# Kernel tuning notes

Hardware: AMD Instinct MI355X
Metric: run time of the kernel (lower is better)

The kernel has to match this reference:

```python
import jax, jax.numpy as jnp
import numpy as np

OUT = 7       # roi_pooling_output_size
SR = 2        # bilinear samples per bin side (torchvision default is adaptive; fixed here)
STRIDES = (4, 8, 16, 32)
LEVELS = (2, 3, 4, 5)  # log2(strides)


def _roi_align(feat, boxes, bidx, scale):
    """roi_align, aligned=False. feat [B,C,H,W], boxes [N,4] xyxy image coords."""
    N = boxes.shape[0]
    C, H, W = feat.shape[1], feat.shape[2], feat.shape[3]
    x1 = boxes[:, 0] * scale; y1 = boxes[:, 1] * scale
    x2 = boxes[:, 2] * scale; y2 = boxes[:, 3] * scale
    rw = jnp.maximum(x2 - x1, 1.0); rh = jnp.maximum(y2 - y1, 1.0)
    g = (jnp.arange(SR, dtype=feat.dtype) + 0.5) / SR
    off = (jnp.arange(OUT, dtype=feat.dtype)[:, None] + g[None, :]).reshape(-1)  # [OUT*SR]
    ys = y1[:, None] + off[None, :] * (rh / OUT)[:, None]  # [N, OUT*SR]
    xs = x1[:, None] + off[None, :] * (rw / OUT)[:, None]
    M = OUT * SR
    y = jnp.broadcast_to(ys[:, :, None], (N, M, M)).reshape(N, M * M)
    x = jnp.broadcast_to(xs[:, None, :], (N, M, M)).reshape(N, M * M)
    valid = (y > -1.0) & (y < H) & (x > -1.0) & (x < W)
    y = jnp.clip(y, 0.0, H - 1); x = jnp.clip(x, 0.0, W - 1)
    y0f = jnp.floor(y); x0f = jnp.floor(x)
    y0 = y0f.astype(jnp.int32); x0 = x0f.astype(jnp.int32)
    yb = jnp.minimum(y0 + 1, H - 1); xb = jnp.minimum(x0 + 1, W - 1)
    ly = y - y0f; lx = x - x0f

    def gat(yi, xi):
        return feat[bidx[:, None], :, yi, xi]  # [N, P, C]

    v = (((1 - ly) * (1 - lx))[..., None] * gat(y0, x0)
         + ((1 - ly) * lx)[..., None] * gat(y0, xb)
         + (ly * (1 - lx))[..., None] * gat(yb, x0)
         + (ly * lx)[..., None] * gat(yb, xb))
    v = jnp.where(valid[..., None], v, 0.0)
    v = v.reshape(N, OUT, SR, OUT, SR, C).mean(axis=(2, 4))  # avg samples per bin
    return v.transpose(0, 3, 1, 2)  # [N, C, OUT, OUT]


def _forward(feat2, feat3, feat4, feat5, rois, W_fc1, b_fc1, W_fc2, b_fc2,
             W_cls, b_cls, W_reg, b_reg):
    feats = (feat2, feat3, feat4, feat5)
    BS, R = rois.shape[0], rois.shape[1]
    N = BS * R
    boxes = rois.reshape(N, 4)
    bidx = jnp.repeat(jnp.arange(BS, dtype=jnp.int32), R)
    w = boxes[:, 2] - boxes[:, 0]
    h = boxes[:, 3] - boxes[:, 1]
    # FPN level routing: floor(4 + log2(sqrt(wh)/224 + 1e-6)); unclamped, as in source
    lv = jnp.floor(4.0 + jnp.log2(jnp.sqrt(w * h) / 224.0 + 1e-6))
    C = feat2.shape[1]
    roi_feats = jnp.zeros((N, C, OUT, OUT), dtype=feat2.dtype)
    for f, s, l in zip(feats, STRIDES, LEVELS):
        rf = _roi_align(f, boxes, bidx, 1.0 / s)
        roi_feats = roi_feats + jnp.where((lv == l)[:, None, None, None], rf, 0.0)
    x = roi_feats.reshape(N, -1)                    # [N, 12544]
    x = jax.nn.relu(x @ W_fc1.T + b_fc1)            # roi_head fc1
    x = jax.nn.relu(x @ W_fc2.T + b_fc2)            # roi_head fc2
    cls_pred = (x @ W_cls.T + b_cls).reshape(BS, R, -1)
    reg_pred = (x @ W_reg.T + b_reg).reshape(BS, R, -1, 4)
    return cls_pred, reg_pred


def setup_inputs() -> dict:
    key = jax.random.key(0)
    ks = jax.random.split(key, 12)
    BS, R, C = 2, 512, 256
    IMG = 800.0
    inp = {}
    for i, (name, s) in enumerate(zip(['feat2', 'feat3', 'feat4', 'feat5'],
                                      [200, 100, 50, 25])):
        inp[name] = jax.random.normal(ks[i], (BS, C, s, s), dtype=jnp.float32)
    # realistic ROIs: uniform centers, log-uniform sizes in [32, 512] px
    ctr = jax.random.uniform(ks[4], (BS, R, 2), minval=0.0, maxval=IMG)
    sz = jnp.exp(jax.random.uniform(ks[5], (BS, R, 2),
                                    minval=jnp.log(32.0), maxval=jnp.log(512.0)))
    x1y1 = jnp.clip(ctr - sz / 2, 0.0, IMG)
    x2y2 = jnp.clip(ctr + sz / 2, 0.0, IMG)
    inp['rois'] = jnp.concatenate([x1y1, x2y2], axis=-1)
    D, F, NCLS = 1024, C * OUT * OUT, 80
    inp['W_fc1'] = 0.01 * jax.random.normal(ks[6], (D, F), dtype=jnp.float32)
    inp['b_fc1'] = jnp.zeros((D,), dtype=jnp.float32)
    inp['W_fc2'] = 0.01 * jax.random.normal(ks[7], (D, D), dtype=jnp.float32)
    inp['b_fc2'] = jnp.zeros((D,), dtype=jnp.float32)
    inp['W_cls'] = 0.01 * jax.random.normal(ks[8], (NCLS + 1, D), dtype=jnp.float32)
    inp['b_cls'] = jnp.zeros((NCLS + 1,), dtype=jnp.float32)
    inp['W_reg'] = 0.01 * jax.random.normal(ks[9], (NCLS * 4, D), dtype=jnp.float32)
    inp['b_reg'] = jnp.zeros((NCLS * 4,), dtype=jnp.float32)
    return inp


def reference(feat2, feat3, feat4, feat5, rois, W_fc1, b_fc1, W_fc2, b_fc2,
              W_cls, b_cls, W_reg, b_reg):
    return _forward(feat2, feat3, feat4, feat5, rois, W_fc1, b_fc1, W_fc2, b_fc2,
                    W_cls, b_cls, W_reg, b_reg)
```

## Files before the change

### kernel.cpp

```cpp
#include <hip/hip_runtime.h>

typedef __bf16 bf16_t;
typedef __bf16 bf16x8 __attribute__((ext_vector_type(8)));
typedef __bf16 bf16x4v __attribute__((ext_vector_type(4)));
typedef float f32x4 __attribute__((ext_vector_type(4)));

#define GLDS16(g, l)                                                            \
  __builtin_amdgcn_global_load_lds((const __attribute__((address_space(1))) void*)(g), \
                                   (__attribute__((address_space(3))) void*)(l), 16, 0, 0)

__global__ __launch_bounds__(256) void prep_all(const float* __restrict__ f2,
                                                const float* __restrict__ f3,
                                                const float* __restrict__ f4,
                                                const float* __restrict__ f5,
                                                const float* __restrict__ W1,
                                                const float* __restrict__ W2,
                                                const float* __restrict__ Wc,
                                                const float* __restrict__ bc,
                                                const float* __restrict__ Wr,
                                                const float* __restrict__ br,
                                                bf16_t* __restrict__ FT2,
                                                bf16_t* __restrict__ FT3,
                                                bf16_t* __restrict__ FT4,
                                                bf16_t* __restrict__ FT5,
                                                bf16_t* __restrict__ W1p,
                                                bf16_t* __restrict__ W2b,
                                                bf16_t* __restrict__ Wcb,
                                                float* __restrict__ bcat) {
  __shared__ __align__(16) char smraw[25344];
  const int bid = blockIdx.x;
  const int t = threadIdx.x;

  if (bid < 6656) {
    float* tile = (float*)smraw;
    const float* src; bf16_t* dst; int P, rel, ptiles;
    if (bid < 5000)      { src = f2; dst = FT2; P = 40000; rel = bid;        ptiles = 625; }
    else if (bid < 6256) { src = f3; dst = FT3; P = 10000; rel = bid - 5000; ptiles = 157; }
    else if (bid < 6576) { src = f4; dst = FT4; P = 2500;  rel = bid - 6256; ptiles = 40; }
    else                 { src = f5; dst = FT5; P = 625;   rel = bid - 6576; ptiles = 10; }
    const int pt = rel % ptiles;
    const int cb = (rel / ptiles) & 3;
    const int b = rel / (ptiles * 4);
    const int p0 = pt * 64, c0 = cb * 64;
    const float* s = src + (size_t)(b * 256 + c0) * P;
#pragma unroll
    for (int it = 0; it < 16; ++it) {
      const int ch = it * 4 + (t >> 6);
      const int px = t & 63;
      float v = 0.0f;
      if (p0 + px < P) v = s[(size_t)ch * P + p0 + px];
      tile[ch * 65 + px] = v;
    }
    __syncthreads();
    bf16_t* d = dst + ((size_t)b * P + p0) * 256 + c0;
#pragma unroll
    for (int it = 0; it < 4; ++it) {
      const int px = it * 16 + (t >> 4);
      const int ch4 = (t & 15) * 4;
      if (p0 + px < P) {
        union { bf16_t bb[4]; uint2 u; } pk;
#pragma unroll
        for (int k2 = 0; k2 < 4; k2++) pk.bb[k2] = (bf16_t)tile[(ch4 + k2) * 65 + px];
        *(uint2*)&d[(size_t)px * 256 + ch4] = pk.u;
      }
    }
  } else if (bid < 7680) {
    bf16_t* pw = (bf16_t*)smraw;
    const int row = bid - 6656;
    const float* src = W1 + (size_t)row * 12544;
    for (int it = 0; it < 49; ++it) {
      const int j = it * 256 + t;
      const int c = j / 49;
      const int bin = j - c * 49;
      pw[bin * 258 + c] = (bf16_t)src[j];
    }
    __syncthreads();
    bf16_t* dst = W1p + (size_t)row * 12544;
    for (int j4 = t; j4 < 3136; j4 += 256) {
      const int bin = j4 >> 6;
      const int c = (j4 & 63) * 4;
      union { bf16_t bb[4]; uint2 u; } pk;
#pragma unroll
      for (int k2 = 0; k2 < 4; k2++) pk.bb[k2] = pw[bin * 258 + c + k2];
      ((uint2*)dst)[j4] = pk.u;
    }
  } else if (bid < 8704) {
    const int i = (bid - 7680) * 256 + t;
    float4 v = ((const float4*)W2)[i];
    union { bf16_t b[4]; uint2 u; } p;
    p.b[0] = (bf16_t)v.x; p.b[1] = (bf16_t)v.y; p.b[2] = (bf16_t)v.z; p.b[3] = (bf16_t)v.w;
    ((uint2*)W2b)[i] = p.u;
  } else {
    const int i = (bid - 8704) * 256 + t;
    const int row = i >> 10, col = i & 1023;
    float v = 0.0f;
    if (row < 81) v = Wc[row * 1024 + col];
    else if (row < 401) v = Wr[(row - 81) * 1024 + col];
    Wcb[i] = (bf16_t)v;
    if (i < 448) bcat[i] = (i < 81) ? bc[i] : ((i < 401) ? br[i - 81] : 0.0f);
  }
}

__global__ __launch_bounds__(256) void roi_align_nhwc(const bf16_t* __restrict__ fb2,
                                                      const bf16_t* __restrict__ fb3,
                                                      const bf16_t* __restrict__ fb4,
                                                      const bf16_t* __restrict__ fb5,
                                                      const float* __restrict__ rois,
                                                      bf16_t* __restrict__ A) {
  const int n = blockIdx.x;
  const int t = threadIdx.x;
  const int b = n >> 9;
  const float4 box = ((const float4*)rois)[n];
  const float w = box.z - box.x, h = box.w - box.y;
  const int lv = (int)floorf(4.0f + log2f(sqrtf(w * h) / 224.0f + 1e-6f));
  bf16_t* Ar = A + (size_t)n * 12544;

  if (lv < 2 || lv > 5) {
    uint2 z; z.x = 0; z.y = 0;
    for (int j = t; j < 3136; j += 256) ((uint2*)Ar)[j] = z;
    return;
  }

  const bf16_t* F; int H, W; float scale;
  if (lv == 2)      { F = fb2; H = 200; W = 200; scale = 0.25f; }
  else if (lv == 3) { F = fb3; H = 100; W = 100; scale = 0.125f; }
  else if (lv == 4) { F = fb4; H = 50;  W = 50;  scale = 0.0625f; }
  else              { F = fb5; H = 25;  W = 25;  scale = 0.03125f; }
  F += (size_t)b * H * W * 256;

  __shared__ int   s_x0[14], s_xb[14], s_y0w[14], s_ybw[14];
  __shared__ float s_wx0[14], s_wx1[14], s_wy0[14], s_wy1[14];

  const float x1s = box.x * scale, y1s = box.y * scale;
  const float x2s = box.z * scale, y2s = box.w * scale;
  const float rw = fmaxf(x2s - x1s, 1.0f), rh = fmaxf(y2s - y1s, 1.0f);
  const float bwx = rw * (1.0f / 7.0f), bwy = rh * (1.0f / 7.0f);

  if (t < 14) {
    const int i2 = t >> 1, j = t & 1;
    const float off = (float)i2 + ((float)j + 0.5f) * 0.5f;
    float x = x1s + off * bwx;
    float vx = (x > -1.0f && x < (float)W) ? 1.0f : 0.0f;
    x = fminf(fmaxf(x, 0.0f), (float)(W - 1));
    float x0f = floorf(x);
    int x0 = (int)x0f;
    s_x0[t] = x0; s_xb[t] = min(x0 + 1, W - 1);
    float lx = x - x0f;
    s_wx0[t] = (1.0f - lx) * vx; s_wx1[t] = lx * vx;
    float y = y1s + off * bwy;
    float vy = (y > -1.0f && y < (float)H) ? 1.0f : 0.0f;
    y = fminf(fmaxf(y, 0.0f), (float)(H - 1));
    float y0f = floorf(y);
    int y0 = (int)y0f;
    s_y0w[t] = y0 * W; s_ybw[t] = min(y0 + 1, H - 1) * W;
    float ly = y - y0f;
    s_wy0[t] = (1.0f - ly) * vy; s_wy1[t] = ly * vy;
  }
  __syncthreads();

  const int wv = t >> 6, l = t & 63;
  const int c4 = l * 4;
  for (int bin = wv; bin < 49; bin += 4) {
    const int by = bin / 7, bx = bin - by * 7;
    float a0 = 0, a1 = 0, a2 = 0, a3 = 0;
#pragma unroll
    for (int sa = 0; sa < 2; sa++) {
      const int my = 2 * by + sa;
      const int y0w = s_y0w[my], ybw = s_ybw[my];
      const float wy0 = s_wy0[my], wy1 = s_wy1[my];
#pragma unroll
      for (int sb = 0; sb < 2; sb++) {
        const int mx = 2 * bx + sb;
        const int x0 = s_x0[mx], xb = s_xb[mx];
        const float w00 = wy0 * s_wx0[mx], w01 = wy0 * s_wx1[mx];
        const float w10 = wy1 * s_wx0[mx], w11 = wy1 * s_wx1[mx];
        bf16x4v v00 = *(const bf16x4v*)&F[(size_t)(y0w + x0) * 256 + c4];
        bf16x4v v01 = *(const bf16x4v*)&F[(size_t)(y0w + xb) * 256 + c4];
        bf16x4v v10 = *(const bf16x4v*)&F[(size_t)(ybw + x0) * 256 + c4];
        bf16x4v v11 = *(const bf16x4v*)&F[(size_t)(ybw + xb) * 256 + c4];
        a0 += w00 * (float)v00[0] + w01 * (float)v01[0] + w10 * (float)v10[0] + w11 * (float)v11[0];
        a1 += w00 * (float)v00[1] + w01 * (float)v01[1] + w10 * (float)v10[1] + w11 * (float)v11[1];
        a2 += w00 * (float)v00[2] + w01 * (float)v01[2] + w10 * (float)v10[2] + w11 * (float)v11[2];
        a3 += w00 * (float)v00[3] + w01 * (float)v01[3] + w10 * (float)v10[3] + w11 * (float)v11[3];
      }
    }
    union { bf16_t bb[4]; uint2 u; } pk;
    pk.bb[0] = (bf16_t)(a0 * 0.25f);
    pk.bb[1] = (bf16_t)(a1 * 0.25f);
    pk.bb[2] = (bf16_t)(a2 * 0.25f);
    pk.bb[3] = (bf16_t)(a3 * 0.25f);
    *(uint2*)&Ar[bin * 256 + c4] = pk.u;
  }
}

__global__ __launch_bounds__(256, 2) void gemm1_splitk(const bf16_t* __restrict__ A,
                                                       const bf16_t* __restrict__ B,
                                                       float* __restrict__ Cp) {
  __shared__ __align__(16) bf16_t As[128 * 32];
  __shared__ __align__(16) bf16_t Bs[128 * 32];
  const int t = threadIdx.x;
  const int w = t >> 6, l = t & 63;
  const int bm = blockIdx.x * 128, bn = blockIdx.y * 128;
  const int K = 12544;
  const int k0 = blockIdx.z * 1568;
  const int row1 = t >> 2;
  const int kc = ((t & 3) ^ ((t >> 3) & 3)) * 8;
  const bf16_t* gA1 = A + (size_t)(bm + row1) * K + k0 + kc;
  const bf16_t* gA2 = gA1 + (size_t)64 * K;
  const bf16_t* gB1 = B + (size_t)(bn + row1) * K + k0 + kc;
  const bf16_t* gB2 = gB1 + (size_t)64 * K;
  bf16_t* lA1 = As + w * 512;
  bf16_t* lA2 = As + 2048 + w * 512;
  bf16_t* lB1 = Bs + w * 512;
  bf16_t* lB2 = Bs + 2048 + w * 512;
  const int wm = (w >> 1) * 64, wn = (w & 1) * 64;
  const int rA = l & 15;
  const int kqs = (((l >> 4) ^ ((rA >> 1) & 3))) * 8;
  f32x4 acc[4][4] = {};

  for (int kk = 0; kk < 49; ++kk) {
    GLDS16(gA1, lA1); GLDS16(gA2, lA2);
    GLDS16(gB1, lB1); GLDS16(gB2, lB2);
    gA1 += 32; gA2 += 32; gB1 += 32; gB2 += 32;
    __syncthreads();
    bf16x8 a[4], b[4];
#pragma unroll
    for (int i = 0; i < 4; i++) {
      a[i] = *(const bf16x8*)&As[(wm + i * 16 + rA) * 32 + kqs];
      b[i] = *(const bf16x8*)&Bs[(wn + i * 16 + rA) * 32 + kqs];
    }
#pragma unroll
    for (int i = 0; i < 4; i++)
#pragma unroll
      for (int j = 0; j < 4; j++)
        acc[i][j] = __builtin_amdgcn_mfma_f32_16x16x32_bf16(a[i], b[j], acc[i][j], 0, 0, 0);
    __syncthreads();
  }

  const int q = l >> 4, cc = l & 15;
  float* Co = Cp + ((size_t)blockIdx.z << 20);
#pragma unroll
  for (int i = 0; i < 4; i++)
#pragma unroll
    for (int j = 0; j < 4; j++) {
      const int col = bn + wn + j * 16 + cc;
      const int r0 = bm + wm + i * 16 + q * 4;
#pragma unroll
      for (int r = 0; r < 4; r++)
        Co[(size_t)(r0 + r) * 1024 + col] = acc[i][j][r];
    }
}

__global__ __launch_bounds__(256) void reduce_fc1(const float* __restrict__ Cp,
                                                  const float* __restrict__ bias,
                                                  bf16_t* __restrict__ X) {
  const int i4 = blockIdx.x * 256 + threadIdx.x;
  const float4* C4 = (const float4*)Cp;
  float4 s = C4[i4];
#pragma unroll
  for (int z = 1; z < 8; z++) {
    float4 v = C4[(size_t)z * 262144 + i4];
    s.x += v.x; s.y += v.y; s.z += v.z; s.w += v.w;
  }
  const float4 bv = *(const float4*)&bias[(i4 & 255) * 4];
  union { bf16_t bb[4]; uint2 u; } pk;
  pk.bb[0] = (bf16_t)fmaxf(s.x + bv.x, 0.0f);
  pk.bb[1] = (bf16_t)fmaxf(s.y + bv.y, 0.0f);
  pk.bb[2] = (bf16_t)fmaxf(s.z + bv.z, 0.0f);
  pk.bb[3] = (bf16_t)fmaxf(s.w + bv.w, 0.0f);
  ((uint2*)X)[i4] = pk.u;
}

template <int MODE>
__global__ __launch_bounds__(256) void gemm_bt(const bf16_t* __restrict__ A,
                                               const bf16_t* __restrict__ B,
                                               const float* __restrict__ bias,
                                               void* __restrict__ out,
                                               int M, int N, int K) {
  __shared__ __align__(16) bf16_t As[64 * 32];
  __shared__ __align__(16) bf16_t Bs[64 * 32];
  const int t = threadIdx.x;
  const int wv = t >> 6, l = t & 63;
  const int bm = blockIdx.x * 64, bn = blockIdx.y * 64;
  const int wm = (wv >> 1) * 32, wn = (wv & 1) * 32;

  const int srow = t >> 2;
  const int skc = (t & 3) * 8;
  const int sst = ((t & 3) ^ ((t >> 3) & 3)) * 8;
  const bf16_t* ga = A + (size_t)(bm + srow) * K + skc;
  const bf16_t* gb = B + (size_t)(bn + srow) * K + skc;

  uint4 ra = *(const uint4*)ga;
  uint4 rb = *(const uint4*)gb;
  f32x4 acc[2][2] = {};

  const int nIter = K >> 5;
  const int rA = l & 15;
  const int kqs = (((l >> 4) ^ ((rA >> 1) & 3))) * 8;
  for (int i = 0; i < nIter; ++i) {
    ga += 32; gb += 32;
    *(uint4*)&As[srow * 32 + sst] = ra;
    *(uint4*)&Bs[srow * 32 + sst] = rb;
    __syncthreads();
    if (i + 1 < nIter) { ra = *(const uint4*)ga; rb = *(const uint4*)gb; }
    bf16x8 a0 = *(const bf16x8*)&As[(wm + rA) * 32 + kqs];
    bf16x8 a1 = *(const bf16x8*)&As[(wm + 16 + rA) * 32 + kqs];
    bf16x8 b0 = *(const bf16x8*)&Bs[(wn + rA) * 32 + kqs];
    bf16x8 b1 = *(const bf16x8*)&Bs[(wn + 16 + rA) * 32 + kqs];
    acc[0][0] = __builtin_amdgcn_mfma_f32_16x16x32_bf16(a0, b0, acc[0][0], 0, 0, 0);
    acc[0][1] = __builtin_amdgcn_mfma_f32_16x16x32_bf16(a0, b1, acc[0][1], 0, 0, 0);
    acc[1][0] = __builtin_amdgcn_mfma_f32_16x16x32_bf16(a1, b0, acc[1][0], 0, 0, 0);
    acc[1][1] = __builtin_amdgcn_mfma_f32_16x16x32_bf16(a1, b1, acc[1][1], 0, 0, 0);
    __syncthreads();
  }

  const int q = l >> 4;
  const int cc = l & 15;
#pragma unroll
  for (int i2 = 0; i2 < 2; i2++) {
#pragma unroll
    for (int j2 = 0; j2 < 2; j2++) {
      const int col = bn + wn + j2 * 16 + cc;
      const int row0 = bm + wm + i2 * 16 + q * 4;
      const float bv = bias[col];
#pragma unroll
      for (int r = 0; r < 4; r++) {
        float v = acc[i2][j2][r] + bv;
        const int row = row0 + r;
        if (MODE == 0) {
          v = fmaxf(v, 0.0f);
          ((bf16_t*)out)[(size_t)row * N + col] = (bf16_t)v;
        } else {
          if (col < 81)       ((float*)out)[(size_t)row * 81 + col] = v;
          else if (col < 401) ((float*)out)[82944 + (size_t)row * 320 + (col - 81)] = v;
        }
      }
    }
  }
}

extern "C" void kernel_launch(void* const* d_in, const int* in_sizes, int n_in,
                              void* d_out, int out_size, void* d_ws, size_t ws_size,
                              hipStream_t stream) {
  const float* f2   = (const float*)d_in[0];
  const float* f3   = (const float*)d_in[1];
  const float* f4   = (const float*)d_in[2];
  const float* f5   = (const float*)d_in[3];
  const float* rois = (const float*)d_in[4];
  const float* W1   = (const float*)d_in[5];
  const float* b1   = (const float*)d_in[6];
  const float* W2   = (const float*)d_in[7];
  const float* b2   = (const float*)d_in[8];
  const float* Wc   = (const float*)d_in[9];
  const float* bc   = (const float*)d_in[10];
  const float* Wr   = (const float*)d_in[11];
  const float* br   = (const float*)d_in[12];

  char* ws = (char*)d_ws;
  bf16_t* Ab   = (bf16_t*)(ws);
  bf16_t* W1b  = (bf16_t*)(ws + 25690112);
  bf16_t* X1b  = (bf16_t*)(ws + 51380224);
  bf16_t* W2b  = (bf16_t*)(ws + 53477376);
  bf16_t* X2b  = (bf16_t*)(ws + 55574528);
  bf16_t* Wcb  = (bf16_t*)(ws + 57671680);
  float*  bcat = (float*)(ws + 58589184);
  bf16_t* FT   = (bf16_t*)(ws + 58591232);
  float*  Cp   = (float*)(ws + 58591232);
  bf16_t* FT2 = FT;
  bf16_t* FT3 = FT + 20480000;
  bf16_t* FT4 = FT + 25600000;
  bf16_t* FT5 = FT + 26880000;

  prep_all<<<10496, 256, 0, stream>>>(f2, f3, f4, f5, W1, W2, Wc, bc, Wr, br,
                                      FT2, FT3, FT4, FT5, W1b, W2b, Wcb, bcat);
  roi_align_nhwc<<<1024, 256, 0, stream>>>(FT2, FT3, FT4, FT5, rois, Ab);
  gemm1_splitk<<<dim3(8, 8, 8), 256, 0, stream>>>(Ab, W1b, Cp);
  reduce_fc1<<<1024, 256, 0, stream>>>(Cp, b1, X1b);
  gemm_bt<0><<<dim3(16, 16), 256, 0, stream>>>(X1b, W2b, b2, (void*)X2b, 1024, 1024, 1024);
  gemm_bt<1><<<dim3(16, 7), 256, 0, stream>>>(X2b, Wcb, bcat, d_out, 1024, 448, 1024);
}
```

Before: 327.0 us.

## Vectorize prep and roi_align loads, split W1 transpose, shrink gemm1 M-tile

```diff
diff --git a/kernel.cpp b/kernel.cpp
--- a/kernel.cpp
+++ b/kernel.cpp
@@ -2,7 +2,6 @@
 
 typedef __bf16 bf16_t;
 typedef __bf16 bf16x8 __attribute__((ext_vector_type(8)));
-typedef __bf16 bf16x4v __attribute__((ext_vector_type(4)));
 typedef float f32x4 __attribute__((ext_vector_type(4)));
 
 #define GLDS16(g, l)                                                            \
@@ -27,7 +26,7 @@
                                                 bf16_t* __restrict__ W2b,
                                                 bf16_t* __restrict__ Wcb,
                                                 float* __restrict__ bcat) {
-  __shared__ __align__(16) char smraw[25344];
+  __shared__ __align__(16) char smraw[16640];
   const int bid = blockIdx.x;
   const int t = threadIdx.x;
 
@@ -43,13 +42,24 @@
     const int b = rel / (ptiles * 4);
     const int p0 = pt * 64, c0 = cb * 64;
     const float* s = src + (size_t)(b * 256 + c0) * P;
-#pragma unroll
-    for (int it = 0; it < 16; ++it) {
-      const int ch = it * 4 + (t >> 6);
-      const int px = t & 63;
-      float v = 0.0f;
-      if (p0 + px < P) v = s[(size_t)ch * P + p0 + px];
-      tile[ch * 65 + px] = v;
+    if (p0 + 64 <= P && (P & 3) == 0) {
+      const int chb = t >> 4, px4 = (t & 15) * 4;
+#pragma unroll
+      for (int it = 0; it < 4; ++it) {
+        const int ch = it * 16 + chb;
+        float4 v = *(const float4*)&s[(size_t)ch * P + p0 + px4];
+        float* tr = &tile[ch * 65 + px4];
+        tr[0] = v.x; tr[1] = v.y; tr[2] = v.z; tr[3] = v.w;
+      }
+    } else {
+#pragma unroll
+      for (int it = 0; it < 16; ++it) {
+        const int ch = it * 4 + (t >> 6);
+        const int px = t & 63;
+        float v = 0.0f;
+        if (p0 + px < P) v = s[(size_t)ch * P + p0 + px];
+        tile[ch * 65 + px] = v;
+      }
     }
     __syncthreads();
     bf16_t* d = dst + ((size_t)b * P + p0) * 256 + c0;
@@ -64,40 +74,44 @@
         *(uint2*)&d[(size_t)px * 256 + ch4] = pk.u;
       }
     }
-  } else if (bid < 7680) {
-    bf16_t* pw = (bf16_t*)smraw;
-    const int row = bid - 6656;
-    const float* src = W1 + (size_t)row * 12544;
-    for (int it = 0; it < 49; ++it) {
-      const int j = it * 256 + t;
-      const int c = j / 49;
-      const int bin = j - c * 49;
-      pw[bin * 258 + c] = (bf16_t)src[j];
-    }
-    __syncthreads();
-    bf16_t* dst = W1p + (size_t)row * 12544;
-    for (int j4 = t; j4 < 3136; j4 += 256) {
-      const int bin = j4 >> 6;
-      const int c = (j4 & 63) * 4;
+  } else if (bid < 8704) {
+    bf16_t* lin = (bf16_t*)smraw;
+    const int idx = bid - 6656;
+    const int row = idx >> 1, c0 = (idx & 1) * 128;
+    const float* src = W1 + (size_t)row * 12544 + (size_t)c0 * 49;
+    for (int i = t; i < 1568; i += 256) {
+      float4 v = ((const float4*)src)[i];
       union { bf16_t bb[4]; uint2 u; } pk;
-#pragma unroll
-      for (int k2 = 0; k2 < 4; k2++) pk.bb[k2] = pw[bin * 258 + c + k2];
-      ((uint2*)dst)[j4] = pk.u;
-    }
-  } else if (bid < 8704) {
-    const int i = (bid - 7680) * 256 + t;
+      pk.bb[0] = (bf16_t)v.x; pk.bb[1] = (bf16_t)v.y;
+      pk.bb[2] = (bf16_t)v.z; pk.bb[3] = (bf16_t)v.w;
+      *(uint2*)&lin[i * 4] = pk.u;
+    }
+    __syncthreads();
+    bf16_t* dst = W1p + (size_t)row * 12544 + c0;
+    for (int j4 = t; j4 < 1568; j4 += 256) {
+      const int bin = j4 >> 5;
+      const int lc = (j4 & 31) * 4;
+      union { bf16_t bb[4]; uint2 u; } pk;
+#pragma unroll
+      for (int k2 = 0; k2 < 4; k2++) pk.bb[k2] = lin[(lc + k2) * 49 + bin];
+      *(uint2*)&dst[bin * 256 + lc] = pk.u;
+    }
+  } else if (bid < 9728) {
+    const int i = (bid - 8704) * 256 + t;
     float4 v = ((const float4*)W2)[i];
     union { bf16_t b[4]; uint2 u; } p;
     p.b[0] = (bf16_t)v.x; p.b[1] = (bf16_t)v.y; p.b[2] = (bf16_t)v.z; p.b[3] = (bf16_t)v.w;
     ((uint2*)W2b)[i] = p.u;
   } else {
-    const int i = (bid - 8704) * 256 + t;
-    const int row = i >> 10, col = i & 1023;
-    float v = 0.0f;
-    if (row < 81) v = Wc[row * 1024 + col];
-    else if (row < 401) v = Wr[(row - 81) * 1024 + col];
-    Wcb[i] = (bf16_t)v;
-    if (i < 448) bcat[i] = (i < 81) ? bc[i] : ((i < 401) ? br[i - 81] : 0.0f);
+    const int q = (bid - 9728) * 256 + t;
+    const int row = q >> 8, col4 = (q & 255) * 4;
+    float4 v = {0.0f, 0.0f, 0.0f, 0.0f};
+    if (row < 81) v = *(const float4*)&Wc[row * 1024 + col4];
+    else if (row < 401) v = *(const float4*)&Wr[(row - 81) * 1024 + col4];
+    union { bf16_t b[4]; uint2 u; } p;
+    p.b[0] = (bf16_t)v.x; p.b[1] = (bf16_t)v.y; p.b[2] = (bf16_t)v.z; p.b[3] = (bf16_t)v.w;
+    ((uint2*)Wcb)[q] = p.u;
+    if (q < 448) bcat[q] = (q < 81) ? bc[q] : ((q < 401) ? br[q - 81] : 0.0f);
   }
 }
 
@@ -116,8 +130,8 @@
   bf16_t* Ar = A + (size_t)n * 12544;
 
   if (lv < 2 || lv > 5) {
-    uint2 z; z.x = 0; z.y = 0;
-    for (int j = t; j < 3136; j += 256) ((uint2*)Ar)[j] = z;
+    uint4 z = {0, 0, 0, 0};
+    for (int j = t; j < 1568; j += 256) ((uint4*)Ar)[j] = z;
     return;
   }
 
@@ -159,10 +173,12 @@
   __syncthreads();
 
   const int wv = t >> 6, l = t & 63;
-  const int c4 = l * 4;
-  for (int bin = wv; bin < 49; bin += 4) {
+  const int half = l >> 5, c8 = (l & 31) * 8;
+  for (int p = wv; p < 25; p += 4) {
+    const int bin = 2 * p + half;
+    if (bin >= 49) continue;
     const int by = bin / 7, bx = bin - by * 7;
-    float a0 = 0, a1 = 0, a2 = 0, a3 = 0;
+    float a[8] = {};
 #pragma unroll
     for (int sa = 0; sa < 2; sa++) {
       const int my = 2 * by + sa;
@@ -174,63 +190,57 @@
         const int x0 = s_x0[mx], xb = s_xb[mx];
         const float w00 = wy0 * s_wx0[mx], w01 = wy0 * s_wx1[mx];
         const float w10 = wy1 * s_wx0[mx], w11 = wy1 * s_wx1[mx];
-        bf16x4v v00 = *(const bf16x4v*)&F[(size_t)(y0w + x0) * 256 + c4];
-        bf16x4v v01 = *(const bf16x4v*)&F[(size_t)(y0w + xb) * 256 + c4];
-        bf16x4v v10 = *(const bf16x4v*)&F[(size_t)(ybw + x0) * 256 + c4];
-        bf16x4v v11 = *(const bf16x4v*)&F[(size_t)(ybw + xb) * 256 + c4];
-        a0 += w00 * (float)v00[0] + w01 * (float)v01[0] + w10 * (float)v10[0] + w11 * (float)v11[0];
-        a1 += w00 * (float)v00[1] + w01 * (float)v01[1] + w10 * (float)v10[1] + w11 * (float)v11[1];
-        a2 += w00 * (float)v00[2] + w01 * (float)v01[2] + w10 * (float)v10[2] + w11 * (float)v11[2];
-        a3 += w00 * (float)v00[3] + w01 * (float)v01[3] + w10 * (float)v10[3] + w11 * (float)v11[3];
-      }
-    }
-    union { bf16_t bb[4]; uint2 u; } pk;
-    pk.bb[0] = (bf16_t)(a0 * 0.25f);
-    pk.bb[1] = (bf16_t)(a1 * 0.25f);
-    pk.bb[2] = (bf16_t)(a2 * 0.25f);
-    pk.bb[3] = (bf16_t)(a3 * 0.25f);
-    *(uint2*)&Ar[bin * 256 + c4] = pk.u;
-  }
-}
-
-__global__ __launch_bounds__(256, 2) void gemm1_splitk(const bf16_t* __restrict__ A,
+        bf16x8 v00 = *(const bf16x8*)&F[(size_t)(y0w + x0) * 256 + c8];
+        bf16x8 v01 = *(const bf16x8*)&F[(size_t)(y0w + xb) * 256 + c8];
+        bf16x8 v10 = *(const bf16x8*)&F[(size_t)(ybw + x0) * 256 + c8];
+        bf16x8 v11 = *(const bf16x8*)&F[(size_t)(ybw + xb) * 256 + c8];
+#pragma unroll
+        for (int k2 = 0; k2 < 8; k2++)
+          a[k2] += w00 * (float)v00[k2] + w01 * (float)v01[k2]
+                 + w10 * (float)v10[k2] + w11 * (float)v11[k2];
+      }
+    }
+    union { bf16_t bb[8]; uint4 u; } pk;
+#pragma unroll
+    for (int k2 = 0; k2 < 8; k2++) pk.bb[k2] = (bf16_t)(a[k2] * 0.25f);
+    *(uint4*)&Ar[bin * 256 + c8] = pk.u;
+  }
+}
+
+__global__ __launch_bounds__(256, 4) void gemm1_splitk(const bf16_t* __restrict__ A,
                                                        const bf16_t* __restrict__ B,
                                                        float* __restrict__ Cp) {
-  __shared__ __align__(16) bf16_t As[128 * 32];
+  __shared__ __align__(16) bf16_t As[64 * 32];
   __shared__ __align__(16) bf16_t Bs[128 * 32];
   const int t = threadIdx.x;
   const int w = t >> 6, l = t & 63;
-  const int bm = blockIdx.x * 128, bn = blockIdx.y * 128;
+  const int bm = blockIdx.x * 64, bn = blockIdx.y * 128;
   const int K = 12544;
   const int k0 = blockIdx.z * 1568;
-  const int row1 = t >> 2;
+  const int row = t >> 2;
   const int kc = ((t & 3) ^ ((t >> 3) & 3)) * 8;
-  const bf16_t* gA1 = A + (size_t)(bm + row1) * K + k0 + kc;
-  const bf16_t* gA2 = gA1 + (size_t)64 * K;
-  const bf16_t* gB1 = B + (size_t)(bn + row1) * K + k0 + kc;
+  const bf16_t* gA  = A + (size_t)(bm + row) * K + k0 + kc;
+  const bf16_t* gB1 = B + (size_t)(bn + row) * K + k0 + kc;
   const bf16_t* gB2 = gB1 + (size_t)64 * K;
-  bf16_t* lA1 = As + w * 512;
-  bf16_t* lA2 = As + 2048 + w * 512;
+  bf16_t* lA  = As + w * 512;
   bf16_t* lB1 = Bs + w * 512;
   bf16_t* lB2 = Bs + 2048 + w * 512;
-  const int wm = (w >> 1) * 64, wn = (w & 1) * 64;
+  const int wm = (w & 1) * 32, wn = (w >> 1) * 64;
   const int rA = l & 15;
   const int kqs = (((l >> 4) ^ ((rA >> 1) & 3))) * 8;
-  f32x4 acc[4][4] = {};
+  f32x4 acc[2][4] = {};
 
   for (int kk = 0; kk < 49; ++kk) {
-    GLDS16(gA1, lA1); GLDS16(gA2, lA2);
-    GLDS16(gB1, lB1); GLDS16(gB2, lB2);
-    gA1 += 32; gA2 += 32; gB1 += 32; gB2 += 32;
-    __syncthreads();
-    bf16x8 a[4], b[4];
-#pragma unroll
-    for (int i = 0; i < 4; i++) {
-      a[i] = *(const bf16x8*)&As[(wm + i * 16 + rA) * 32 + kqs];
-      b[i] = *(const bf16x8*)&Bs[(wn + i * 16 + rA) * 32 + kqs];
-    }
-#pragma unroll
-    for (int i = 0; i < 4; i++)
+    GLDS16(gA, lA); GLDS16(gB1, lB1); GLDS16(gB2, lB2);
+    gA += 32; gB1 += 32; gB2 += 32;
+    __syncthreads();
+    bf16x8 a[2], b[4];
+#pragma unroll
+    for (int i = 0; i < 2; i++) a[i] = *(const bf16x8*)&As[(wm + i * 16 + rA) * 32 + kqs];
+#pragma unroll
+    for (int j = 0; j < 4; j++) b[j] = *(const bf16x8*)&Bs[(wn + j * 16 + rA) * 32 + kqs];
+#pragma unroll
+    for (int i = 0; i < 2; i++)
 #pragma unroll
       for (int j = 0; j < 4; j++)
         acc[i][j] = __builtin_amdgcn_mfma_f32_16x16x32_bf16(a[i], b[j], acc[i][j], 0, 0, 0);
@@ -240,7 +250,7 @@
   const int q = l >> 4, cc = l & 15;
   float* Co = Cp + ((size_t)blockIdx.z << 20);
 #pragma unroll
-  for (int i = 0; i < 4; i++)
+  for (int i = 0; i < 2; i++)
 #pragma unroll
     for (int j = 0; j < 4; j++) {
       const int col = bn + wn + j * 16 + cc;
@@ -371,10 +381,10 @@
   bf16_t* FT4 = FT + 25600000;
   bf16_t* FT5 = FT + 26880000;
 
-  prep_all<<<10496, 256, 0, stream>>>(f2, f3, f4, f5, W1, W2, Wc, bc, Wr, br,
+  prep_all<<<10176, 256, 0, stream>>>(f2, f3, f4, f5, W1, W2, Wc, bc, Wr, br,
                                       FT2, FT3, FT4, FT5, W1b, W2b, Wcb, bcat);
   roi_align_nhwc<<<1024, 256, 0, stream>>>(FT2, FT3, FT4, FT5, rois, Ab);
-  gemm1_splitk<<<dim3(8, 8, 8), 256, 0, stream>>>(Ab, W1b, Cp);
+  gemm1_splitk<<<dim3(16, 8, 8), 256, 0, stream>>>(Ab, W1b, Cp);
   reduce_fc1<<<1024, 256, 0, stream>>>(Cp, b1, X1b);
   gemm_bt<0><<<dim3(16, 16), 256, 0, stream>>>(X1b, W2b, b2, (void*)X2b, 1024, 1024, 1024);
   gemm_bt<1><<<dim3(16, 7), 256, 0, stream>>>(X2b, Wcb, bcat, d_out, 1024, 448, 1024);
```

Measured after the change: 323.2 us. Within noise of the previous version (-1.2%).
